# Kernel optimization log

Measured on AMD Instinct MI355X. Metric: run time of the kernel, lower is better.

Reference implementation:

```python
import jax, jax.numpy as jnp
import numpy as np

AB = 8            # activation quant bits
NOISE_LEVEL = 0.1
CY_SCALE = 2.0    # stands in for args.cy_scale
B, IN, H = 8192, 512, 512


def _fake_quant(x, bits, sign):
    # forward: clip/clamp then round-to-grid; backward (STE) handled elsewhere
    if sign:
        delta = 1.0 / (2.0 ** (bits - 1))
        xc = jnp.clip(x, -1.0 + delta, 1.0 - delta)
        scale = 2.0 ** (bits - 1)
    else:
        xc = jnp.clip(x, 0.0, 1.0)
        scale = 2.0 ** bits
    q = jnp.round(xc * scale) / scale
    # STE: identity gradient w.r.t. x
    return x + jax.lax.stop_gradient(q - x)


def setup_inputs() -> dict:
    key = jax.random.key(0)
    ks = jax.random.split(key, 11)
    return {
        "input": jax.random.normal(ks[0], (B, IN), jnp.float32),
        "hx": jax.random.normal(ks[1], (B, H), jnp.float32),
        "cx": jax.random.normal(ks[2], (B, H), jnp.float32),
        "weight_ih": jax.random.normal(ks[3], (4 * H, IN), jnp.float32),
        "weight_hh": jax.random.normal(ks[4], (4 * H, H), jnp.float32),
        "bias_ih": jax.random.normal(ks[5], (4 * H,), jnp.float32),
        "bias_hh": jax.random.normal(ks[6], (4 * H,), jnp.float32),
        "noise_ih": jax.random.normal(ks[7], (IN, 4 * H), jnp.float32),
        "noise_hh": jax.random.normal(ks[8], (H, 4 * H), jnp.float32),
        "noise_bias_ih": jax.random.normal(ks[9], (4 * H,), jnp.float32),
        "noise_bias_hh": jax.random.normal(ks[10], (4 * H,), jnp.float32),
    }


def reference(input, hx, cx, weight_ih, weight_hh, bias_ih, bias_hh,
              noise_ih, noise_hh, noise_bias_ih, noise_bias_hh):
    # noisy weights: noise = randn * w.max() * noise_level (raw randn passed in)
    w_ih = weight_ih.T + noise_ih * (jnp.max(weight_ih) * NOISE_LEVEL)   # [IN,4H]
    w_hh = weight_hh.T + noise_hh * (jnp.max(weight_hh) * NOISE_LEVEL)   # [H,4H]
    b_ih = bias_ih + noise_bias_ih * (jnp.max(bias_ih) * NOISE_LEVEL)
    b_hh = bias_hh + noise_bias_hh * (jnp.max(bias_hh) * NOISE_LEVEL)

    gates = input @ w_ih + b_ih + hx @ w_hh + b_hh                        # [B,4H]
    ingate, forgetgate, cellgate, outgate = jnp.split(gates, 4, axis=1)

    ingate = _fake_quant(jax.nn.sigmoid(ingate), AB, False)
    forgetgate = _fake_quant(jax.nn.sigmoid(forgetgate), AB, False)
    cellgate = _fake_quant(jnp.tanh(cellgate), AB, True)
    outgate = _fake_quant(jax.nn.sigmoid(outgate), AB, False)

    cy = _fake_quant(
        (_fake_quant(forgetgate * cx, AB, True)
         + _fake_quant(ingate * cellgate, AB, True)) / CY_SCALE,
        AB, True)
    hy = _fake_quant(
        outgate * _fake_quant(jnp.tanh(cy * CY_SCALE), AB, True),
        AB, True)
    return (hy, cy)
```

## Files before the change

kernel.cpp:

```cpp
#include <hip/hip_runtime.h>
#include <cstdint>

typedef unsigned short u16;
typedef __bf16 bf16x8 __attribute__((ext_vector_type(8)));
typedef float f32x4 __attribute__((ext_vector_type(4)));

#define NB 8192
#define HD 512
#define KD 1024
#define ND 2048
#define HY_OFF (NB * HD)
#define NT 32

__device__ __forceinline__ u16 f2bf(float f) {
  unsigned u = __float_as_uint(f);
  u += 0x7FFFu + ((u >> 16) & 1u);
  return (u16)(u >> 16);
}
__device__ __forceinline__ float bf2f(u16 h) {
  return __uint_as_float(((unsigned)h) << 16);
}
__device__ __forceinline__ void atomicMaxF(float* a, float v) {
  if (v >= 0.f) atomicMax((int*)a, __float_as_int(v));
  else          atomicMin((unsigned int*)a, __float_as_uint(v));
}
__device__ __forceinline__ float fq_u(float x) {
  float xc = fminf(fmaxf(x, 0.0f), 1.0f);
  return rintf(xc * 256.0f) * (1.0f / 256.0f);
}
__device__ __forceinline__ float fq_s(float x) {
  const float lim = 1.0f - 1.0f / 128.0f;
  float xc = fminf(fmaxf(x, -lim), lim);
  return rintf(xc * 128.0f) * (1.0f / 128.0f);
}
__device__ __forceinline__ float sigm(float x) { return 1.0f / (1.0f + expf(-x)); }

__device__ __forceinline__ void gload_lds16(const u16* g, u16* l) {
  __builtin_amdgcn_global_load_lds(
      (const __attribute__((address_space(1))) void*)g,
      (__attribute__((address_space(3))) void*)l, 16, 0, 0);
}

__global__ __launch_bounds__(256) void k_prep_max(
    const float* __restrict__ w_ih, const float* __restrict__ w_hh,
    const float* __restrict__ b_ih, const float* __restrict__ b_hh,
    float* __restrict__ maxes) {
  int bid = blockIdx.x;
  const float* src; int slot, base;
  if (bid < 1024)      { src = w_ih; slot = 0; base = bid * 1024; }
  else if (bid < 2048) { src = w_hh; slot = 1; base = (bid - 1024) * 1024; }
  else if (bid < 2050) { src = b_ih; slot = 2; base = (bid - 2048) * 1024; }
  else                 { src = b_hh; slot = 3; base = (bid - 2050) * 1024; }
  float m = -INFINITY;
  for (int i = threadIdx.x; i < 1024; i += 256) m = fmaxf(m, src[base + i]);
  for (int k = 1; k < 64; k <<= 1) m = fmaxf(m, __shfl_xor(m, k, 64));
  __shared__ float sm[4];
  if ((threadIdx.x & 63) == 0) sm[threadIdx.x >> 6] = m;
  __syncthreads();
  if (threadIdx.x == 0) {
    m = fmaxf(fmaxf(sm[0], sm[1]), fmaxf(sm[2], sm[3]));
    atomicMaxF(&maxes[slot], m);
  }
}

__global__ __launch_bounds__(256) void k_prep_build(
    const float* __restrict__ input, const float* __restrict__ hx,
    const float* __restrict__ w_ih, const float* __restrict__ w_hh,
    const float* __restrict__ n_ih, const float* __restrict__ n_hh,
    const float* __restrict__ b_ih, const float* __restrict__ b_hh,
    const float* __restrict__ nb_ih, const float* __restrict__ nb_hh,
    const float* __restrict__ maxes,
    u16* __restrict__ Xhi, u16* __restrict__ Xlo,
    u16* __restrict__ Whi, u16* __restrict__ Wlo,
    float* __restrict__ biasC) {
  const int bid = blockIdx.x;
  if (bid < 2048) {
    const int total4 = NB * KD / 4;
    for (int e4 = bid * 256 + threadIdx.x; e4 < total4; e4 += 2048 * 256) {
      int row = e4 >> 8;
      int c4  = e4 & 255;
      float4 v = (c4 < 128)
          ? reinterpret_cast<const float4*>(input)[row * 128 + c4]
          : reinterpret_cast<const float4*>(hx)[row * 128 + (c4 - 128)];
      float xs[4] = {v.x, v.y, v.z, v.w};
      ushort4 hi, lo;
      u16 h0 = f2bf(xs[0]); u16 l0 = f2bf(xs[0] - bf2f(h0));
      u16 h1 = f2bf(xs[1]); u16 l1 = f2bf(xs[1] - bf2f(h1));
      u16 h2 = f2bf(xs[2]); u16 l2 = f2bf(xs[2] - bf2f(h2));
      u16 h3 = f2bf(xs[3]); u16 l3 = f2bf(xs[3] - bf2f(h3));
      hi.x = h0; hi.y = h1; hi.z = h2; hi.w = h3;
      lo.x = l0; lo.y = l1; lo.z = l2; lo.w = l3;
      reinterpret_cast<ushort4*>(Xhi)[e4] = hi;
      reinterpret_cast<ushort4*>(Xlo)[e4] = lo;
    }
  } else if (bid < 2560) {
    __shared__ float nT[256][17];
    const int w  = bid - 2048;
    const int cg = w >> 2, kb = w & 3;
    const int j0 = cg * 16;
    const int g  = ((j0 >> 7) & 1) * 2 + ((j0 >> 4) & 1);
    const int hb = ((j0 >> 8) << 2) | ((j0 >> 5) & 3);
    const int col0 = g * 512 + (hb << 4);
    const int k0 = kb * 256;
    {
      const int cl = threadIdx.x & 15;
      const int kr = threadIdx.x >> 4;
#pragma unroll 4
      for (int i = 0; i < 16; ++i) {
        const int k = k0 + kr + 16 * i;
        nT[kr + 16 * i][cl] = (k < 512) ? n_ih[k * ND + col0 + cl]
                                        : n_hh[(k - 512) * ND + col0 + cl];
      }
    }
    __syncthreads();
    const float s_ih = maxes[0] * 0.1f, s_hh = maxes[1] * 0.1f;
    const int c  = threadIdx.x >> 4;
    const int kl = threadIdx.x & 15;
    const int colL = col0 + c;
    const int j = j0 + c;
#pragma unroll
    for (int kk = 0; kk < 4; ++kk) {
      const int k = k0 + kk * 64 + kl * 4;
      float4 wv; float s;
      if (k < 512) {
        wv = reinterpret_cast<const float4*>(w_ih)[(colL * 512 + k) >> 2];
        s = s_ih;
      } else {
        wv = reinterpret_cast<const float4*>(w_hh)[(colL * 512 + k - 512) >> 2];
        s = s_hh;
      }
      const int kt = k - k0;
      float xs[4] = {wv.x + nT[kt + 0][c] * s, wv.y + nT[kt + 1][c] * s,
                     wv.z + nT[kt + 2][c] * s, wv.w + nT[kt + 3][c] * s};
      ushort4 hi, lo;
      u16 h0 = f2bf(xs[0]); u16 l0 = f2bf(xs[0] - bf2f(h0));
      u16 h1 = f2bf(xs[1]); u16 l1 = f2bf(xs[1] - bf2f(h1));
      u16 h2 = f2bf(xs[2]); u16 l2 = f2bf(xs[2] - bf2f(h2));
      u16 h3 = f2bf(xs[3]); u16 l3 = f2bf(xs[3] - bf2f(h3));
      hi.x = h0; hi.y = h1; hi.z = h2; hi.w = h3;
      lo.x = l0; lo.y = l1; lo.z = l2; lo.w = l3;
      reinterpret_cast<ushort4*>(Whi)[(j * KD + k) >> 2] = hi;
      reinterpret_cast<ushort4*>(Wlo)[(j * KD + k) >> 2] = lo;
    }
  } else {
    int j = (bid - 2560) * 256 + threadIdx.x;
    if (j < ND) {
      int g  = ((j >> 7) & 1) * 2 + ((j >> 4) & 1);
      int hb = ((j >> 8) << 2) | ((j >> 5) & 3);
      int col = g * 512 + (hb << 4) + (j & 15);
      biasC[j] = b_ih[col] + nb_ih[col] * (maxes[2] * 0.1f)
               + b_hh[col] + nb_hh[col] * (maxes[3] * 0.1f);
    }
  }
}

__global__ __launch_bounds__(512, 2) void k_gemm_lstm(
    const u16* __restrict__ Xhi, const u16* __restrict__ Xlo,
    const u16* __restrict__ Whi, const u16* __restrict__ Wlo,
    const float* __restrict__ biasC, const float* __restrict__ cx,
    float* __restrict__ out) {
  __shared__ u16 L[2][4][8192];
  const int tid  = threadIdx.x;
  const int lane = tid & 63, wid = tid >> 6;
  const int wr = wid >> 2, wc = wid & 3;
  const int lr = lane & 15, lg = lane >> 4;
  const int xcd = blockIdx.x & 7, tt = blockIdx.x >> 3;
  const int bm = ((xcd >> 1) << 3) | (tt & 7);
  const int bn = ((xcd & 1) << 2) | (tt >> 3);
  const int mbase = bm * 256, nbase = bn * 256;

  const int l8 = lane >> 3, l7 = lane & 7;
  const int csrc  = l7 ^ l8;
  const int srow  = wid * 16 + 2 * l8 + (csrc >> 2);
  const int skoff = (csrc & 3) * 8;
  const int sdst  = wid * 512;

  const int fro = (lr >> 1) * 64 + ((((lr & 1) << 2) | lg) ^ ((lr >> 1) & 7)) * 8;

  f32x4 acc[8][4] = {};
  bf16x8 afr[4][2];
  bf16x8 bfr[2][2][2];

#define STAGE(V, SLOT, BUF, HALF)                                             \
  {                                                                           \
    const u16* arr_ = (BUF) == 0 ? Xhi : (BUF) == 1 ? Xlo                     \
                      : (BUF) == 2 ? Whi : Wlo;                               \
    const int gb_ = ((BUF) < 2 ? mbase : nbase) + (HALF) * 128 + srow;        \
    gload_lds16(arr_ + (size_t)gb_ * KD + (V) * 32 + skoff,                   \
                &L[(SLOT)][(BUF)][(HALF) * 4096 + sdst]);                     \
  }

#define STAGE8(V, SLOT)                                                       \
  {                                                                           \
    STAGE(V, SLOT, 0, 0); STAGE(V, SLOT, 1, 0);                               \
    STAGE(V, SLOT, 2, 0); STAGE(V, SLOT, 3, 0);                               \
    STAGE(V, SLOT, 2, 1); STAGE(V, SLOT, 3, 1);                               \
    STAGE(V, SLOT, 0, 1); STAGE(V, SLOT, 1, 1);                               \
  }

#define RD_A(S, MH)                                                           \
  _Pragma("unroll") for (int m2 = 0; m2 < 4; ++m2) {                          \
    const int ab = ((MH) * 128 + wr * 64 + m2 * 16) * 32 + fro;               \
    afr[m2][0] = *reinterpret_cast<const bf16x8*>(&L[S][0][ab]);              \
    afr[m2][1] = *reinterpret_cast<const bf16x8*>(&L[S][1][ab]);              \
  }

#define RD_B2(S)                                                              \
  _Pragma("unroll") for (int nh = 0; nh < 2; ++nh)                            \
    _Pragma("unroll") for (int n2 = 0; n2 < 2; ++n2) {                        \
      const int bb = (nh * 128 + wc * 32 + n2 * 16) * 32 + fro;               \
      bfr[nh][n2][0] = *reinterpret_cast<const bf16x8*>(&L[S][2][bb]);        \
      bfr[nh][n2][1] = *reinterpret_cast<const bf16x8*>(&L[S][3][bb]);        \
    }

#define MM(MH, NH)                                                            \
  {                                                                           \
    __builtin_amdgcn_s_setprio(1);                                            \
    _Pragma("unroll") for (int t = 0; t < 3; ++t)                             \
      _Pragma("unroll") for (int m2 = 0; m2 < 4; ++m2)                        \
        _Pragma("unroll") for (int n2 = 0; n2 < 2; ++n2) {                    \
          f32x4* ac = &acc[(MH) * 4 + m2][(NH) * 2 + n2];                     \
          *ac = __builtin_amdgcn_mfma_f32_16x16x32_bf16(afr[m2][t == 1],      \
                    bfr[(NH)][n2][t == 2], *ac, 0, 0, 0);                     \
        }                                                                     \
    __builtin_amdgcn_s_setprio(0);                                            \
  }

#define TILE(U, S)                                                            \
  STAGE8((U) + 1, (S) ^ 1)                                                    \
  RD_B2(S)                                                                    \
  RD_A(S, 0)                                                                  \
  MM(0, 0) MM(0, 1)                                                           \
  RD_A(S, 1)                                                                  \
  MM(1, 1) MM(1, 0)                                                           \
  __syncthreads();

  STAGE8(0, 0)
  __syncthreads();

  for (int u = 0; u < NT - 2; u += 2) {
    TILE(u, 0)
    TILE(u + 1, 1)
  }
  TILE(30, 0)
  RD_B2(1)
  RD_A(1, 0)
  MM(0, 0) MM(0, 1)
  RD_A(1, 1)
  MM(1, 1) MM(1, 0)

#undef TILE
#undef MM
#undef RD_B2
#undef RD_A
#undef STAGE8
#undef STAGE

  const int hb = bn * 4 + wc;
  const int h = hb * 16 + lr;
  float bias[4];
#pragma unroll
  for (int g = 0; g < 4; ++g)
    bias[g] = biasC[bn * 256 + ((g >> 1) * 8 + wc * 2 + (g & 1)) * 16 + lr];
#pragma unroll
  for (int mh = 0; mh < 2; ++mh) {
#pragma unroll
    for (int m2 = 0; m2 < 4; ++m2) {
      const int m = mh * 4 + m2;
#pragma unroll
      for (int r = 0; r < 4; ++r) {
        const int row = mbase + mh * 128 + wr * 64 + m2 * 16 + lg * 4 + r;
        const float gi = acc[m][0][r] + bias[0];
        const float gf = acc[m][1][r] + bias[1];
        const float gc = acc[m][2][r] + bias[2];
        const float go = acc[m][3][r] + bias[3];
        const float ig = fq_u(sigm(gi));
        const float fg = fq_u(sigm(gf));
        const float cg = fq_s(tanhf(gc));
        const float og = fq_u(sigm(go));
        const float cxv = cx[(size_t)row * HD + h];
        const float t1 = fq_s(fg * cxv);
        const float t2 = fq_s(ig * cg);
        const float cyv = fq_s((t1 + t2) * 0.5f);
        const float hyv = fq_s(og * fq_s(tanhf(cyv * 2.0f)));
        out[(size_t)row * HD + h] = hyv;
        out[HY_OFF + (size_t)row * HD + h] = cyv;
      }
    }
  }
}

extern "C" void kernel_launch(void* const* d_in, const int* in_sizes, int n_in,
                              void* d_out, int out_size, void* d_ws, size_t ws_size,
                              hipStream_t stream) {
  const float* input = (const float*)d_in[0];
  const float* hx    = (const float*)d_in[1];
  const float* cx    = (const float*)d_in[2];
  const float* w_ih  = (const float*)d_in[3];
  const float* w_hh  = (const float*)d_in[4];
  const float* b_ih  = (const float*)d_in[5];
  const float* b_hh  = (const float*)d_in[6];
  const float* n_ih  = (const float*)d_in[7];
  const float* n_hh  = (const float*)d_in[8];
  const float* nb_ih = (const float*)d_in[9];
  const float* nb_hh = (const float*)d_in[10];
  float* out = (float*)d_out;

  char* ws = (char*)d_ws;
  float* maxes = (float*)ws;
  u16* Xhi = (u16*)(ws + 256);
  u16* Xlo = (u16*)(ws + 256 + 16777216);
  u16* Whi = (u16*)(ws + 256 + 2 * 16777216);
  u16* Wlo = (u16*)(ws + 256 + 2 * 16777216 + 4194304);
  float* biasC = (float*)(ws + 256 + 2 * 16777216 + 2 * 4194304);

  hipMemsetAsync(maxes, 0xFF, 16, stream);
  hipLaunchKernelGGL(k_prep_max, dim3(2052), dim3(256), 0, stream,
                     w_ih, w_hh, b_ih, b_hh, maxes);
  hipLaunchKernelGGL(k_prep_build, dim3(2568), dim3(256), 0, stream,
                     input, hx, w_ih, w_hh, n_ih, n_hh, b_ih, b_hh,
                     nb_ih, nb_hh, maxes, Xhi, Xlo, Whi, Wlo, biasC);
  hipLaunchKernelGGL(k_gemm_lstm, dim3(256), dim3(512), 0, stream,
                     Xhi, Xlo, Whi, Wlo, biasC, cx, out);
}
```

Before: 147.6 us.

## Pipeline split-bf16 GEMM with fine-grained phased LDS staging and merge prep launches

The GEMM main loop is restructured into eight phases per pair of K steps. Each phase issues a half-tile async global-to-LDS load for a future step alongside MFMA work, using explicit waitcnt and raw barriers instead of full syncthreads. The three split-precision products are recast as a longer K loop over hi/hi, lo/hi and hi/lo segments with a new 64-wide swizzled LDS layout. The prep is reorganised so that the activation bf16 split runs in the same launch as the weight max reduction. Hand-placed waitcnts are fragile and risk races if the counts are wrong.

```diff
diff --git a/kernel.cpp b/kernel.cpp
--- a/kernel.cpp
+++ b/kernel.cpp
@@ -10,7 +10,6 @@
 #define KD 1024
 #define ND 2048
 #define HY_OFF (NB * HD)
-#define NT 32
 
 __device__ __forceinline__ u16 f2bf(float f) {
   unsigned u = __float_as_uint(f);
@@ -41,38 +40,11 @@
       (__attribute__((address_space(3))) void*)l, 16, 0, 0);
 }
 
-__global__ __launch_bounds__(256) void k_prep_max(
+__global__ __launch_bounds__(256) void k_prep1(
+    const float* __restrict__ input, const float* __restrict__ hx,
     const float* __restrict__ w_ih, const float* __restrict__ w_hh,
     const float* __restrict__ b_ih, const float* __restrict__ b_hh,
-    float* __restrict__ maxes) {
-  int bid = blockIdx.x;
-  const float* src; int slot, base;
-  if (bid < 1024)      { src = w_ih; slot = 0; base = bid * 1024; }
-  else if (bid < 2048) { src = w_hh; slot = 1; base = (bid - 1024) * 1024; }
-  else if (bid < 2050) { src = b_ih; slot = 2; base = (bid - 2048) * 1024; }
-  else                 { src = b_hh; slot = 3; base = (bid - 2050) * 1024; }
-  float m = -INFINITY;
-  for (int i = threadIdx.x; i < 1024; i += 256) m = fmaxf(m, src[base + i]);
-  for (int k = 1; k < 64; k <<= 1) m = fmaxf(m, __shfl_xor(m, k, 64));
-  __shared__ float sm[4];
-  if ((threadIdx.x & 63) == 0) sm[threadIdx.x >> 6] = m;
-  __syncthreads();
-  if (threadIdx.x == 0) {
-    m = fmaxf(fmaxf(sm[0], sm[1]), fmaxf(sm[2], sm[3]));
-    atomicMaxF(&maxes[slot], m);
-  }
-}
-
-__global__ __launch_bounds__(256) void k_prep_build(
-    const float* __restrict__ input, const float* __restrict__ hx,
-    const float* __restrict__ w_ih, const float* __restrict__ w_hh,
-    const float* __restrict__ n_ih, const float* __restrict__ n_hh,
-    const float* __restrict__ b_ih, const float* __restrict__ b_hh,
-    const float* __restrict__ nb_ih, const float* __restrict__ nb_hh,
-    const float* __restrict__ maxes,
-    u16* __restrict__ Xhi, u16* __restrict__ Xlo,
-    u16* __restrict__ Whi, u16* __restrict__ Wlo,
-    float* __restrict__ biasC) {
+    u16* __restrict__ Xhi, u16* __restrict__ Xlo, float* __restrict__ maxes) {
   const int bid = blockIdx.x;
   if (bid < 2048) {
     const int total4 = NB * KD / 4;
@@ -93,10 +65,37 @@
       reinterpret_cast<ushort4*>(Xhi)[e4] = hi;
       reinterpret_cast<ushort4*>(Xlo)[e4] = lo;
     }
-  } else if (bid < 2560) {
+  } else {
+    int mb = bid - 2048;
+    const float* src; int slot, base;
+    if (mb < 1024)      { src = w_ih; slot = 0; base = mb * 1024; }
+    else if (mb < 2048) { src = w_hh; slot = 1; base = (mb - 1024) * 1024; }
+    else if (mb < 2050) { src = b_ih; slot = 2; base = (mb - 2048) * 1024; }
+    else                { src = b_hh; slot = 3; base = (mb - 2050) * 1024; }
+    float m = -INFINITY;
+    for (int i = threadIdx.x; i < 1024; i += 256) m = fmaxf(m, src[base + i]);
+    for (int k = 1; k < 64; k <<= 1) m = fmaxf(m, __shfl_xor(m, k, 64));
+    __shared__ float sm[4];
+    if ((threadIdx.x & 63) == 0) sm[threadIdx.x >> 6] = m;
+    __syncthreads();
+    if (threadIdx.x == 0) {
+      m = fmaxf(fmaxf(sm[0], sm[1]), fmaxf(sm[2], sm[3]));
+      atomicMaxF(&maxes[slot], m);
+    }
+  }
+}
+
+__global__ __launch_bounds__(256) void k_prep2(
+    const float* __restrict__ w_ih, const float* __restrict__ w_hh,
+    const float* __restrict__ n_ih, const float* __restrict__ n_hh,
+    const float* __restrict__ b_ih, const float* __restrict__ b_hh,
+    const float* __restrict__ nb_ih, const float* __restrict__ nb_hh,
+    const float* __restrict__ maxes,
+    u16* __restrict__ Whi, u16* __restrict__ Wlo, float* __restrict__ biasC) {
+  const int bid = blockIdx.x;
+  if (bid < 512) {
     __shared__ float nT[256][17];
-    const int w  = bid - 2048;
-    const int cg = w >> 2, kb = w & 3;
+    const int cg = bid >> 2, kb = bid & 3;
     const int j0 = cg * 16;
     const int g  = ((j0 >> 7) & 1) * 2 + ((j0 >> 4) & 1);
     const int hb = ((j0 >> 8) << 2) | ((j0 >> 5) & 3);
@@ -143,7 +142,7 @@
       reinterpret_cast<ushort4*>(Wlo)[(j * KD + k) >> 2] = lo;
     }
   } else {
-    int j = (bid - 2560) * 256 + threadIdx.x;
+    int j = (bid - 512) * 256 + threadIdx.x;
     if (j < ND) {
       int g  = ((j >> 7) & 1) * 2 + ((j >> 4) & 1);
       int hb = ((j >> 8) << 2) | ((j >> 5) & 3);
@@ -159,102 +158,117 @@
     const u16* __restrict__ Whi, const u16* __restrict__ Wlo,
     const float* __restrict__ biasC, const float* __restrict__ cx,
     float* __restrict__ out) {
-  __shared__ u16 L[2][4][8192];
+  __shared__ u16 L[2][2][2][8192];
   const int tid  = threadIdx.x;
   const int lane = tid & 63, wid = tid >> 6;
   const int wr = wid >> 2, wc = wid & 3;
   const int lr = lane & 15, lg = lane >> 4;
+  const int l7 = lane & 7, l8 = lane >> 3;
   const int xcd = blockIdx.x & 7, tt = blockIdx.x >> 3;
   const int bm = ((xcd >> 1) << 3) | (tt & 7);
   const int bn = ((xcd & 1) << 2) | (tt >> 3);
   const int mbase = bm * 256, nbase = bn * 256;
 
-  const int l8 = lane >> 3, l7 = lane & 7;
-  const int csrc  = l7 ^ l8;
-  const int srow  = wid * 16 + 2 * l8 + (csrc >> 2);
-  const int skoff = (csrc & 3) * 8;
-  const int sdst  = wid * 512;
-
-  const int fro = (lr >> 1) * 64 + ((((lr & 1) << 2) | lg) ^ ((lr >> 1) & 7)) * 8;
+  const int csrc = (l7 ^ l8) * 8;
 
   f32x4 acc[8][4] = {};
   bf16x8 afr[4][2];
   bf16x8 bfr[2][2][2];
 
-#define STAGE(V, SLOT, BUF, HALF)                                             \
+#define STAGEH(V, SLOT, AB, HALF)                                             \
   {                                                                           \
-    const u16* arr_ = (BUF) == 0 ? Xhi : (BUF) == 1 ? Xlo                     \
-                      : (BUF) == 2 ? Whi : Wlo;                               \
-    const int gb_ = ((BUF) < 2 ? mbase : nbase) + (HALF) * 128 + srow;        \
-    gload_lds16(arr_ + (size_t)gb_ * KD + (V) * 32 + skoff,                   \
-                &L[(SLOT)][(BUF)][(HALF) * 4096 + sdst]);                     \
-  }
-
-#define STAGE8(V, SLOT)                                                       \
-  {                                                                           \
-    STAGE(V, SLOT, 0, 0); STAGE(V, SLOT, 1, 0);                               \
-    STAGE(V, SLOT, 2, 0); STAGE(V, SLOT, 3, 0);                               \
-    STAGE(V, SLOT, 2, 1); STAGE(V, SLOT, 3, 1);                               \
-    STAGE(V, SLOT, 0, 1); STAGE(V, SLOT, 1, 1);                               \
+    const int v_ = (V);                                                       \
+    const int seg_ = v_ >> 4;                                                 \
+    const u16* src_ = (AB) ? ((seg_ == 2) ? Wlo : Whi)                        \
+                           : ((seg_ == 1) ? Xlo : Xhi);                       \
+    const int kk_ = (v_ & 15) << 6;                                           \
+    const int pb_ = ((AB) ? nbase : mbase) + (HALF) * 128;                    \
+    gload_lds16(src_ + (size_t)(pb_ + wid * 8 + l8) * KD + kk_ + csrc,        \
+                &L[SLOT][AB][HALF][(wid * 8) * 64]);                          \
+    gload_lds16(src_ + (size_t)(pb_ + 64 + wid * 8 + l8) * KD + kk_ + csrc,   \
+                &L[SLOT][AB][HALF][(64 + wid * 8) * 64]);                     \
   }
 
 #define RD_A(S, MH)                                                           \
   _Pragma("unroll") for (int m2 = 0; m2 < 4; ++m2) {                          \
-    const int ab = ((MH) * 128 + wr * 64 + m2 * 16) * 32 + fro;               \
-    afr[m2][0] = *reinterpret_cast<const bf16x8*>(&L[S][0][ab]);              \
-    afr[m2][1] = *reinterpret_cast<const bf16x8*>(&L[S][1][ab]);              \
-  }
-
-#define RD_B2(S)                                                              \
-  _Pragma("unroll") for (int nh = 0; nh < 2; ++nh)                            \
-    _Pragma("unroll") for (int n2 = 0; n2 < 2; ++n2) {                        \
-      const int bb = (nh * 128 + wc * 32 + n2 * 16) * 32 + fro;               \
-      bfr[nh][n2][0] = *reinterpret_cast<const bf16x8*>(&L[S][2][bb]);        \
-      bfr[nh][n2][1] = *reinterpret_cast<const bf16x8*>(&L[S][3][bb]);        \
-    }
-
-#define MM(MH, NH)                                                            \
+    const int rb_ = (wr * 64 + m2 * 16 + lr) * 64;                            \
+    afr[m2][0] = *reinterpret_cast<const bf16x8*>(                            \
+        &L[S][0][MH][rb_ + ((0 + lg) ^ (lr & 7)) * 8]);                       \
+    afr[m2][1] = *reinterpret_cast<const bf16x8*>(                            \
+        &L[S][0][MH][rb_ + ((4 + lg) ^ (lr & 7)) * 8]);                       \
+  }
+
+#define RD_B(S, NH)                                                           \
+  _Pragma("unroll") for (int n2 = 0; n2 < 2; ++n2) {                          \
+    const int rb_ = (wc * 32 + n2 * 16 + lr) * 64;                            \
+    bfr[(NH)][n2][0] = *reinterpret_cast<const bf16x8*>(                      \
+        &L[S][1][NH][rb_ + ((0 + lg) ^ (lr & 7)) * 8]);                       \
+    bfr[(NH)][n2][1] = *reinterpret_cast<const bf16x8*>(                      \
+        &L[S][1][NH][rb_ + ((4 + lg) ^ (lr & 7)) * 8]);                       \
+  }
+
+#define LG8 asm volatile("s_waitcnt lgkmcnt(8)" ::: "memory")
+#define VM6 asm volatile("s_waitcnt vmcnt(6)" ::: "memory")
+#define VM8 asm volatile("s_waitcnt vmcnt(8)" ::: "memory")
+#define VM0 asm volatile("s_waitcnt vmcnt(0)" ::: "memory")
+
+#define PH(S, MH, NH, RA, RB, STG, W12, WVM)                                  \
   {                                                                           \
+    if (RA) { RD_A(S, MH) }                                                   \
+    if (RB) { RD_B(S, NH) }                                                   \
+    STG;                                                                      \
+    W12;                                                                      \
+    WVM;                                                                      \
+    __builtin_amdgcn_s_barrier();                                             \
+    asm volatile("s_waitcnt lgkmcnt(0)" ::: "memory");                        \
+    __builtin_amdgcn_sched_barrier(0);                                        \
     __builtin_amdgcn_s_setprio(1);                                            \
-    _Pragma("unroll") for (int t = 0; t < 3; ++t)                             \
+    _Pragma("unroll") for (int ks = 0; ks < 2; ++ks)                          \
       _Pragma("unroll") for (int m2 = 0; m2 < 4; ++m2)                        \
         _Pragma("unroll") for (int n2 = 0; n2 < 2; ++n2) {                    \
           f32x4* ac = &acc[(MH) * 4 + m2][(NH) * 2 + n2];                     \
-          *ac = __builtin_amdgcn_mfma_f32_16x16x32_bf16(afr[m2][t == 1],      \
-                    bfr[(NH)][n2][t == 2], *ac, 0, 0, 0);                     \
+          *ac = __builtin_amdgcn_mfma_f32_16x16x32_bf16(                      \
+              afr[m2][ks], bfr[(NH)][n2][ks], *ac, 0, 0, 0);                  \
         }                                                                     \
     __builtin_amdgcn_s_setprio(0);                                            \
-  }
-
-#define TILE(U, S)                                                            \
-  STAGE8((U) + 1, (S) ^ 1)                                                    \
-  RD_B2(S)                                                                    \
-  RD_A(S, 0)                                                                  \
-  MM(0, 0) MM(0, 1)                                                           \
-  RD_A(S, 1)                                                                  \
-  MM(1, 1) MM(1, 0)                                                           \
-  __syncthreads();
-
-  STAGE8(0, 0)
-  __syncthreads();
-
-  for (int u = 0; u < NT - 2; u += 2) {
-    TILE(u, 0)
-    TILE(u + 1, 1)
-  }
-  TILE(30, 0)
-  RD_B2(1)
-  RD_A(1, 0)
-  MM(0, 0) MM(0, 1)
-  RD_A(1, 1)
-  MM(1, 1) MM(1, 0)
-
-#undef TILE
-#undef MM
-#undef RD_B2
+    __builtin_amdgcn_s_barrier();                                             \
+  }
+
+  STAGEH(0, 0, 0, 0); STAGEH(0, 0, 1, 0); STAGEH(0, 0, 1, 1); STAGEH(0, 0, 0, 1);
+  STAGEH(1, 1, 0, 0); STAGEH(1, 1, 1, 0); STAGEH(1, 1, 1, 1); STAGEH(1, 1, 0, 1);
+  VM8;
+  __builtin_amdgcn_s_barrier();
+
+#pragma unroll 1
+  for (int i = 0; i < 23; ++i) {
+    const int T = 2 * i;
+    PH(0, 0, 0, 1, 1, , LG8, )
+    PH(0, 0, 1, 0, 1, STAGEH(T + 2, 0, 0, 0), , )
+    PH(0, 1, 1, 1, 0, STAGEH(T + 2, 0, 1, 0), , )
+    PH(0, 1, 0, 0, 0, STAGEH(T + 2, 0, 1, 1), , VM6)
+    PH(1, 0, 0, 1, 1, STAGEH(T + 2, 0, 0, 1), LG8, )
+    PH(1, 0, 1, 0, 1, STAGEH(T + 3, 1, 0, 0), , )
+    PH(1, 1, 1, 1, 0, STAGEH(T + 3, 1, 1, 0), , )
+    PH(1, 1, 0, 0, 0,
+       { STAGEH(T + 3, 1, 1, 1); STAGEH(T + 3, 1, 0, 1); }, , VM8)
+  }
+  PH(0, 0, 0, 1, 1, , LG8, )
+  PH(0, 0, 1, 0, 1, , , )
+  PH(0, 1, 1, 1, 0, , , )
+  PH(0, 1, 0, 0, 0, , , VM0)
+  PH(1, 0, 0, 1, 1, , LG8, )
+  PH(1, 0, 1, 0, 1, , , )
+  PH(1, 1, 1, 1, 0, , , )
+  PH(1, 1, 0, 0, 0, , , )
+
+#undef PH
+#undef VM0
+#undef VM8
+#undef VM6
+#undef LG8
+#undef RD_B
 #undef RD_A
-#undef STAGE8
-#undef STAGE
+#undef STAGEH
 
   const int hb = bn * 4 + wc;
   const int h = hb * 16 + lr;
@@ -315,11 +329,11 @@
   float* biasC = (float*)(ws + 256 + 2 * 16777216 + 2 * 4194304);
 
   hipMemsetAsync(maxes, 0xFF, 16, stream);
-  hipLaunchKernelGGL(k_prep_max, dim3(2052), dim3(256), 0, stream,
-                     w_ih, w_hh, b_ih, b_hh, maxes);
-  hipLaunchKernelGGL(k_prep_build, dim3(2568), dim3(256), 0, stream,
-                     input, hx, w_ih, w_hh, n_ih, n_hh, b_ih, b_hh,
-                     nb_ih, nb_hh, maxes, Xhi, Xlo, Whi, Wlo, biasC);
+  hipLaunchKernelGGL(k_prep1, dim3(4100), dim3(256), 0, stream,
+                     input, hx, w_ih, w_hh, b_ih, b_hh, Xhi, Xlo, maxes);
+  hipLaunchKernelGGL(k_prep2, dim3(520), dim3(256), 0, stream,
+                     w_ih, w_hh, n_ih, n_hh, b_ih, b_hh, nb_ih, nb_hh,
+                     maxes, Whi, Wlo, biasC);
   hipLaunchKernelGGL(k_gemm_lstm, dim3(256), dim3(512), 0, stream,
                      Xhi, Xlo, Whi, Wlo, biasC, cx, out);
 }
```

Result: no change. 148.6 us (+0.7%).
